# Performance work log

Measured on AMD Instinct MI355X. Metric: run time of the kernel, lower is better.

The kernel has to match this reference:

```python
import jax, jax.numpy as jnp
import numpy as np

N_NODES = 10000
N_EDGES = 320000
D = 128      # node/edge feature dim
H = 512      # MLP hidden width


def _mlp(x, W1, b1, W2, b2):
    return jax.nn.relu(x @ W1 + b1) @ W2 + b2


def setup_inputs() -> dict:
    key = jax.random.key(0)
    ks = jax.random.split(key, 8)
    s = lambda fan_in: 1.0 / np.sqrt(fan_in)
    return {
        "x": jax.random.normal(ks[0], (N_NODES, D), jnp.float32),
        "edge_index": jax.random.randint(ks[1], (2, N_EDGES), 0, N_NODES, jnp.int64),
        "edge_attr": jax.random.normal(ks[2], (N_EDGES, D), jnp.float32),
        "We1": jax.random.normal(ks[3], (3 * D, H), jnp.float32) * s(3 * D),
        "be1": jnp.zeros((H,), jnp.float32),
        "We2": jax.random.normal(ks[4], (H, D), jnp.float32) * s(H),
        "be2": jnp.zeros((D,), jnp.float32),
        "Wn1": jax.random.normal(ks[5], (2 * D, H), jnp.float32) * s(2 * D),
        "bn1": jnp.zeros((H,), jnp.float32),
        "Wn2": jax.random.normal(ks[6], (H, D), jnp.float32) * s(H),
        "bn2": jnp.zeros((D,), jnp.float32),
    }


def reference(x, edge_index, edge_attr, We1, be1, We2, be2, Wn1, bn1, Wn2, bn2):
    senders = edge_index[0]
    receivers = edge_index[1]
    # gather -> edge MLP
    edge_inputs = jnp.concatenate([x[senders], x[receivers], edge_attr], axis=-1)  # [E, 3D]
    updated_edge_attr = _mlp(edge_inputs, We1, be1, We2, be2)                      # [E, D]
    # scatter-add into receiving nodes
    aggregated = jax.ops.segment_sum(updated_edge_attr, receivers, num_segments=x.shape[0])  # [N, D]
    # node MLP
    node_inputs = jnp.concatenate([x, aggregated], axis=-1)                        # [N, 2D]
    updated_nodes = _mlp(node_inputs, Wn1, bn1, Wn2, bn2)                          # [N, D]
    return updated_nodes, updated_edge_attr
```

## Files before the change

### kernel.cpp

```cpp
#include <hip/hip_runtime.h>
#include <hip/hip_bf16.h>

#define N_NODES 10000
#define N_EDGES 320000
#define D 128
#define H 512

typedef __bf16 bf16x8 __attribute__((ext_vector_type(8)));
typedef float f32x4 __attribute__((ext_vector_type(4)));
typedef unsigned short u16x8 __attribute__((ext_vector_type(8)));

__device__ __forceinline__ unsigned short f2bf(float f) {
    union { float f; unsigned u; } v; v.f = f;
    unsigned r = v.u + 0x7fffu + ((v.u >> 16) & 1u);
    return (unsigned short)(r >> 16);
}

__global__ void cast_x_kernel(const float* __restrict__ x, unsigned short* __restrict__ xb) {
    int t = blockIdx.x * 256 + threadIdx.x;
    float4 v = reinterpret_cast<const float4*>(x)[t];
    ushort4 o;
    o.x = f2bf(v.x); o.y = f2bf(v.y); o.z = f2bf(v.z); o.w = f2bf(v.w);
    reinterpret_cast<ushort4*>(xb)[t] = o;
}

__global__ void swizzle_w_kernel(const float* __restrict__ W, unsigned short* __restrict__ out,
                                 int K, int Nn) {
    int t = blockIdx.x * 256 + threadIdx.x;
    int total = (K >> 5) * (Nn >> 4) * 64;
    if (t >= total) return;
    int lane = t & 63;
    int tile = t >> 6;
    int ntiles = Nn >> 4;
    int nt = tile % ntiles;
    int kt = tile / ntiles;
    int k0 = kt * 32 + (lane >> 4) * 8;
    int n  = nt * 16 + (lane & 15);
    unsigned short tmp[8];
#pragma unroll
    for (int j = 0; j < 8; ++j) tmp[j] = f2bf(W[(size_t)(k0 + j) * Nn + n]);
    ushort4* dst = reinterpret_cast<ushort4*>(out + (size_t)t * 8);
    dst[0] = *reinterpret_cast<ushort4*>(&tmp[0]);
    dst[1] = *reinterpret_cast<ushort4*>(&tmp[4]);
}

__global__ void hist_kernel(const int* __restrict__ eidx, int* __restrict__ deg) {
    int e = blockIdx.x * 256 + threadIdx.x;
    if (e < N_EDGES) atomicAdd(&deg[eidx[N_EDGES + e]], 1);
}

__global__ __launch_bounds__(1024) void scan_kernel(const int* __restrict__ deg,
                                                    int* __restrict__ rowstart,
                                                    int* __restrict__ cursor) {
    __shared__ int wsums[16];
    const int t = threadIdx.x;
    const int lane = t & 63, wv = t >> 6;
    const int base = t * 10;
    int loc[10];
    int s = 0;
#pragma unroll
    for (int i = 0; i < 10; ++i) {
        int v = (base + i < N_NODES) ? deg[base + i] : 0;
        loc[i] = s; s += v;
    }
    const int tot = s;
    int inc = tot;
#pragma unroll
    for (int d = 1; d < 64; d <<= 1) {
        int n = __shfl_up(inc, d, 64);
        if (lane >= d) inc += n;
    }
    if (lane == 63) wsums[wv] = inc;
    __syncthreads();
    if (t == 0) {
        int run = 0;
#pragma unroll
        for (int w = 0; w < 16; ++w) { int v = wsums[w]; wsums[w] = run; run += v; }
    }
    __syncthreads();
    const int off = wsums[wv] + inc - tot;
#pragma unroll
    for (int i = 0; i < 10; ++i) {
        int idx = base + i;
        if (idx < N_NODES) { int v = off + loc[i]; rowstart[idx] = v; cursor[idx] = v; }
    }
    if (t == 1023) rowstart[N_NODES] = off + tot;
}

__global__ void scatter_kernel(const int* __restrict__ eidx, int* __restrict__ cursor,
                               int* __restrict__ elist) {
    int e = blockIdx.x * 256 + threadIdx.x;
    if (e < N_EDGES) {
        int p = atomicAdd(&cursor[eidx[N_EDGES + e]], 1);
        elist[p] = e;
    }
}

__global__ __launch_bounds__(256, 2) void edge_mlp_kernel(
    const unsigned short* __restrict__ xb,
    const int* __restrict__ eidx,
    const float* __restrict__ edge_attr,
    const unsigned short* __restrict__ We1s,
    const float* __restrict__ be1,
    const unsigned short* __restrict__ We2s,
    const float* __restrict__ be2,
    float* __restrict__ out_edges)
{
    __shared__ unsigned short sA[64 * 392];
    __shared__ unsigned short sH[64 * 136];

    const int tid = threadIdx.x;
    const int wave = tid >> 6, lane = tid & 63;
    const int e0 = blockIdx.x * 64;
    const int l15 = lane & 15;
    const int q8 = (lane >> 4) * 8;

#pragma unroll
    for (int seg = 0; seg < 2; ++seg) {
        for (int c = tid; c < 1024; c += 256) {
            int row = c >> 4;
            int off = (c & 15) << 3;
            int e = e0 + row;
            int node = eidx[seg * N_EDGES + e];
            *reinterpret_cast<bf16x8*>(&sA[row * 392 + seg * 128 + off]) =
                *reinterpret_cast<const bf16x8*>(&xb[(size_t)node * 128 + off]);
        }
    }
    for (int c = tid; c < 1024; c += 256) {
        int row = c >> 4;
        int off = (c & 15) << 3;
        int e = e0 + row;
        const float4* src = reinterpret_cast<const float4*>(&edge_attr[(size_t)e * 128 + off]);
        float4 v0 = src[0], v1 = src[1];
        u16x8 o;
        o[0] = f2bf(v0.x); o[1] = f2bf(v0.y); o[2] = f2bf(v0.z); o[3] = f2bf(v0.w);
        o[4] = f2bf(v1.x); o[5] = f2bf(v1.y); o[6] = f2bf(v1.z); o[7] = f2bf(v1.w);
        *reinterpret_cast<u16x8*>(&sA[row * 392 + 256 + off]) = o;
    }
    __syncthreads();

    f32x4 acc1[8][4];
#pragma unroll
    for (int j = 0; j < 8; ++j)
#pragma unroll
        for (int mt = 0; mt < 4; ++mt) acc1[j][mt] = (f32x4){0.f, 0.f, 0.f, 0.f};
    f32x4 acc2[2][4];
#pragma unroll
    for (int nn = 0; nn < 2; ++nn)
#pragma unroll
        for (int mt = 0; mt < 4; ++mt) acc2[nn][mt] = (f32x4){0.f, 0.f, 0.f, 0.f};

#pragma unroll 2
    for (int kt = 0; kt < 12; ++kt) {
        bf16x8 a[4];
#pragma unroll
        for (int mt = 0; mt < 4; ++mt)
            a[mt] = *reinterpret_cast<const bf16x8*>(&sA[(mt * 16 + l15) * 392 + kt * 32 + q8]);
#pragma unroll
        for (int j = 0; j < 8; ++j) {
            int ntile = (j >> 1) * 8 + wave * 2 + (j & 1);
            bf16x8 b = *reinterpret_cast<const bf16x8*>(
                &We1s[(((size_t)kt * 32 + ntile) * 64 + lane) * 8]);
#pragma unroll
            for (int mt = 0; mt < 4; ++mt)
                acc1[j][mt] = __builtin_amdgcn_mfma_f32_16x16x32_bf16(a[mt], b, acc1[j][mt], 0, 0, 0);
        }
    }

#pragma unroll
    for (int h = 0; h < 4; ++h) {
        __syncthreads();
#pragma unroll
        for (int nn = 0; nn < 2; ++nn) {
            int cc = (wave * 2 + nn) * 16 + l15;
            float bias = be1[h * 128 + cc];
#pragma unroll
            for (int mt = 0; mt < 4; ++mt)
#pragma unroll
                for (int r = 0; r < 4; ++r) {
                    float v = acc1[h * 2 + nn][mt][r] + bias;
                    v = v > 0.f ? v : 0.f;
                    int row = mt * 16 + (lane >> 4) * 4 + r;
                    sH[row * 136 + cc] = f2bf(v);
                }
        }
        __syncthreads();

#pragma unroll
        for (int kt = 0; kt < 4; ++kt) {
            bf16x8 a[4];
#pragma unroll
            for (int mt = 0; mt < 4; ++mt)
                a[mt] = *reinterpret_cast<const bf16x8*>(&sH[(mt * 16 + l15) * 136 + kt * 32 + q8]);
#pragma unroll
            for (int nn = 0; nn < 2; ++nn) {
                int ntile = wave * 2 + nn;
                bf16x8 b = *reinterpret_cast<const bf16x8*>(
                    &We2s[(((size_t)(h * 4 + kt) * 8 + ntile) * 64 + lane) * 8]);
#pragma unroll
                for (int mt = 0; mt < 4; ++mt)
                    acc2[nn][mt] = __builtin_amdgcn_mfma_f32_16x16x32_bf16(a[mt], b, acc2[nn][mt], 0, 0, 0);
            }
        }
    }

#pragma unroll
    for (int nn = 0; nn < 2; ++nn) {
        int cc = (wave * 2 + nn) * 16 + l15;
        float bias = be2[cc];
#pragma unroll
        for (int mt = 0; mt < 4; ++mt)
#pragma unroll
            for (int r = 0; r < 4; ++r) {
                int row = mt * 16 + (lane >> 4) * 4 + r;
                out_edges[(size_t)(e0 + row) * 128 + cc] = acc2[nn][mt][r] + bias;
            }
    }
}

__global__ __launch_bounds__(256, 2) void node_mlp_kernel(
    const unsigned short* __restrict__ xb,
    const float* __restrict__ out_edges,
    const int* __restrict__ rowstart,
    const int* __restrict__ elist,
    const unsigned short* __restrict__ Wn1s,
    const float* __restrict__ bn1,
    const unsigned short* __restrict__ Wn2s,
    const float* __restrict__ bn2,
    float* __restrict__ out_nodes)
{
    __shared__ unsigned short sA[64 * 264];
    __shared__ unsigned short sH[64 * 136];

    const int tid = threadIdx.x;
    const int wave = tid >> 6, lane = tid & 63;
    const int n0 = blockIdx.x * 64;
    const int l15 = lane & 15;
    const int q8 = (lane >> 4) * 8;

    for (int c = tid; c < 1024; c += 256) {
        int row = c >> 4;
        int off = (c & 15) << 3;
        int node = n0 + row;
        bf16x8 v = {};
        if (node < N_NODES)
            v = *reinterpret_cast<const bf16x8*>(&xb[(size_t)node * 128 + off]);
        *reinterpret_cast<bf16x8*>(&sA[row * 264 + off]) = v;
    }

    {
        int row = tid >> 2, chunk = tid & 3;
        int node = n0 + row;
        f32x4 ag[8];
#pragma unroll
        for (int q = 0; q < 8; ++q) ag[q] = (f32x4){0.f, 0.f, 0.f, 0.f};
        if (node < N_NODES) {
            int r0 = rowstart[node], r1 = rowstart[node + 1];
            for (int j = r0; j < r1; ++j) {
                int e = elist[j];
                const f32x4* src =
                    reinterpret_cast<const f32x4*>(&out_edges[(size_t)e * 128 + chunk * 32]);
#pragma unroll
                for (int q = 0; q < 8; ++q) ag[q] += src[q];
            }
        }
#pragma unroll
        for (int q = 0; q < 4; ++q) {
            u16x8 o;
            o[0] = f2bf(ag[2 * q][0]); o[1] = f2bf(ag[2 * q][1]);
            o[2] = f2bf(ag[2 * q][2]); o[3] = f2bf(ag[2 * q][3]);
            o[4] = f2bf(ag[2 * q + 1][0]); o[5] = f2bf(ag[2 * q + 1][1]);
            o[6] = f2bf(ag[2 * q + 1][2]); o[7] = f2bf(ag[2 * q + 1][3]);
            *reinterpret_cast<u16x8*>(&sA[row * 264 + 128 + chunk * 32 + q * 8]) = o;
        }
    }
    __syncthreads();

    f32x4 acc1[8][4];
#pragma unroll
    for (int j = 0; j < 8; ++j)
#pragma unroll
        for (int mt = 0; mt < 4; ++mt) acc1[j][mt] = (f32x4){0.f, 0.f, 0.f, 0.f};
    f32x4 acc2[2][4];
#pragma unroll
    for (int nn = 0; nn < 2; ++nn)
#pragma unroll
        for (int mt = 0; mt < 4; ++mt) acc2[nn][mt] = (f32x4){0.f, 0.f, 0.f, 0.f};

#pragma unroll 2
    for (int kt = 0; kt < 8; ++kt) {
        bf16x8 a[4];
#pragma unroll
        for (int mt = 0; mt < 4; ++mt)
            a[mt] = *reinterpret_cast<const bf16x8*>(&sA[(mt * 16 + l15) * 264 + kt * 32 + q8]);
#pragma unroll
        for (int j = 0; j < 8; ++j) {
            int ntile = (j >> 1) * 8 + wave * 2 + (j & 1);
            bf16x8 b = *reinterpret_cast<const bf16x8*>(
                &Wn1s[(((size_t)kt * 32 + ntile) * 64 + lane) * 8]);
#pragma unroll
            for (int mt = 0; mt < 4; ++mt)
                acc1[j][mt] = __builtin_amdgcn_mfma_f32_16x16x32_bf16(a[mt], b, acc1[j][mt], 0, 0, 0);
        }
    }

#pragma unroll
    for (int h = 0; h < 4; ++h) {
        __syncthreads();
#pragma unroll
        for (int nn = 0; nn < 2; ++nn) {
            int cc = (wave * 2 + nn) * 16 + l15;
            float bias = bn1[h * 128 + cc];
#pragma unroll
            for (int mt = 0; mt < 4; ++mt)
#pragma unroll
                for (int r = 0; r < 4; ++r) {
                    float v = acc1[h * 2 + nn][mt][r] + bias;
                    v = v > 0.f ? v : 0.f;
                    int row = mt * 16 + (lane >> 4) * 4 + r;
                    sH[row * 136 + cc] = f2bf(v);
                }
        }
        __syncthreads();

#pragma unroll
        for (int kt = 0; kt < 4; ++kt) {
            bf16x8 a[4];
#pragma unroll
            for (int mt = 0; mt < 4; ++mt)
                a[mt] = *reinterpret_cast<const bf16x8*>(&sH[(mt * 16 + l15) * 136 + kt * 32 + q8]);
#pragma unroll
            for (int nn = 0; nn < 2; ++nn) {
                int ntile = wave * 2 + nn;
                bf16x8 b = *reinterpret_cast<const bf16x8*>(
                    &Wn2s[(((size_t)(h * 4 + kt) * 8 + ntile) * 64 + lane) * 8]);
#pragma unroll
                for (int mt = 0; mt < 4; ++mt)
                    acc2[nn][mt] = __builtin_amdgcn_mfma_f32_16x16x32_bf16(a[mt], b, acc2[nn][mt], 0, 0, 0);
            }
        }
    }

#pragma unroll
    for (int nn = 0; nn < 2; ++nn) {
        int cc = (wave * 2 + nn) * 16 + l15;
        float bias = bn2[cc];
#pragma unroll
        for (int mt = 0; mt < 4; ++mt)
#pragma unroll
            for (int r = 0; r < 4; ++r) {
                int row = mt * 16 + (lane >> 4) * 4 + r;
                int node = n0 + row;
                if (node < N_NODES)
                    out_nodes[(size_t)node * 128 + cc] = acc2[nn][mt][r] + bias;
            }
    }
}

extern "C" void kernel_launch(void* const* d_in, const int* in_sizes, int n_in,
                              void* d_out, int out_size, void* d_ws, size_t ws_size,
                              hipStream_t stream) {
    const float* x         = (const float*)d_in[0];
    const int*   eidx      = (const int*)d_in[1];
    const float* edge_attr = (const float*)d_in[2];
    const float* We1       = (const float*)d_in[3];
    const float* be1       = (const float*)d_in[4];
    const float* We2       = (const float*)d_in[5];
    const float* be2       = (const float*)d_in[6];
    const float* Wn1       = (const float*)d_in[7];
    const float* bn1       = (const float*)d_in[8];
    const float* Wn2       = (const float*)d_in[9];
    const float* bn2       = (const float*)d_in[10];
    float* out = (float*)d_out;

    char* ws = (char*)d_ws;
    size_t off = 0;
    auto alloc = [&](size_t bytes) {
        void* p = ws + off;
        off += (bytes + 255) & ~(size_t)255;
        return p;
    };
    unsigned short* xb   = (unsigned short*)alloc((size_t)N_NODES * D * 2);
    unsigned short* We1s = (unsigned short*)alloc((size_t)384 * 512 * 2);
    unsigned short* We2s = (unsigned short*)alloc((size_t)512 * 128 * 2);
    unsigned short* Wn1s = (unsigned short*)alloc((size_t)256 * 512 * 2);
    unsigned short* Wn2s = (unsigned short*)alloc((size_t)512 * 128 * 2);
    int* deg      = (int*)alloc((size_t)(N_NODES + 1) * 4);
    int* rowstart = (int*)alloc((size_t)(N_NODES + 1) * 4);
    int* cursor   = (int*)alloc((size_t)(N_NODES + 1) * 4);
    int* elist    = (int*)alloc((size_t)N_EDGES * 4);

    float* out_edges = out + (size_t)N_NODES * D;

    hipMemsetAsync(deg, 0, (size_t)N_NODES * sizeof(int), stream);
    cast_x_kernel<<<(N_NODES * D / 4 + 255) / 256, 256, 0, stream>>>(x, xb);
    swizzle_w_kernel<<<(12 * 32 * 64 + 255) / 256, 256, 0, stream>>>(We1, We1s, 384, 512);
    swizzle_w_kernel<<<(16 * 8 * 64 + 255) / 256, 256, 0, stream>>>(We2, We2s, 512, 128);
    swizzle_w_kernel<<<(8 * 32 * 64 + 255) / 256, 256, 0, stream>>>(Wn1, Wn1s, 256, 512);
    swizzle_w_kernel<<<(16 * 8 * 64 + 255) / 256, 256, 0, stream>>>(Wn2, Wn2s, 512, 128);

    hist_kernel<<<(N_EDGES + 255) / 256, 256, 0, stream>>>(eidx, deg);
    scan_kernel<<<1, 1024, 0, stream>>>(deg, rowstart, cursor);
    scatter_kernel<<<(N_EDGES + 255) / 256, 256, 0, stream>>>(eidx, cursor, elist);

    edge_mlp_kernel<<<N_EDGES / 64, 256, 0, stream>>>(
        xb, eidx, edge_attr, We1s, be1, We2s, be2, out_edges);
    node_mlp_kernel<<<(N_NODES + 63) / 64, 256, 0, stream>>>(
        xb, out_edges, rowstart, elist, Wn1s, bn1, Wn2s, bn2, out);
}
```

Baseline: 685.0 us.

## Double-buffer hidden tile in reused LDS and split aggregation into separate kernel

The edge and node MLP kernels now reuse the input tile's shared memory as two ping-pong hidden buffers. The ReLU write of the next hidden chunk overlaps with the second GEMM on the current chunk, which removes one barrier per chunk and lowers LDS use per block. The segment-sum aggregation moves out of the node MLP into a dedicated kernel with one wave per node. That kernel writes bf16 aggregates, which fixes the poor parallelism of the old four-threads-per-node gather, at the cost of an extra launch and an intermediate buffer.

```diff
diff --git a/kernel.cpp b/kernel.cpp
--- a/kernel.cpp
+++ b/kernel.cpp
@@ -96,6 +96,25 @@
     }
 }
 
+__global__ __launch_bounds__(256) void agg_kernel(
+    const float* __restrict__ out_edges,
+    const int* __restrict__ rowstart,
+    const int* __restrict__ elist,
+    unsigned short* __restrict__ aggb)
+{
+    int node = blockIdx.x * 4 + (threadIdx.x >> 6);
+    int lane = threadIdx.x & 63;
+    int r0 = rowstart[node], r1 = rowstart[node + 1];
+    float sx = 0.f, sy = 0.f;
+    for (int j = r0; j < r1; ++j) {
+        int e = elist[j];
+        float2 v = *reinterpret_cast<const float2*>(&out_edges[(size_t)e * 128 + lane * 2]);
+        sx += v.x; sy += v.y;
+    }
+    ushort2 o; o.x = f2bf(sx); o.y = f2bf(sy);
+    *reinterpret_cast<ushort2*>(&aggb[(size_t)node * 128 + lane * 2]) = o;
+}
+
 __global__ __launch_bounds__(256, 2) void edge_mlp_kernel(
     const unsigned short* __restrict__ xb,
     const int* __restrict__ eidx,
@@ -107,7 +126,8 @@
     float* __restrict__ out_edges)
 {
     __shared__ unsigned short sA[64 * 392];
-    __shared__ unsigned short sH[64 * 136];
+    unsigned short* const sH0 = sA;
+    unsigned short* const sH1 = sA + 64 * 136;
 
     const int tid = threadIdx.x;
     const int wave = tid >> 6, lane = tid & 63;
@@ -167,41 +187,56 @@
         }
     }
 
+#define WRITE_H(hh, dst, B1)                                                  \
+    {                                                                         \
+        _Pragma("unroll")                                                     \
+        for (int nn = 0; nn < 2; ++nn) {                                      \
+            int cc = (wave * 2 + nn) * 16 + l15;                              \
+            float bias = (B1)[(hh) * 128 + cc];                               \
+            _Pragma("unroll")                                                 \
+            for (int mt = 0; mt < 4; ++mt)                                    \
+                _Pragma("unroll")                                             \
+                for (int r = 0; r < 4; ++r) {                                 \
+                    float v = acc1[(hh) * 2 + nn][mt][r] + bias;              \
+                    v = v > 0.f ? v : 0.f;                                    \
+                    int row = mt * 16 + (lane >> 4) * 4 + r;                  \
+                    (dst)[row * 136 + cc] = f2bf(v);                          \
+                }                                                             \
+        }                                                                     \
+    }
+
+#define GEMM2_CHUNK(hh, src, W2)                                              \
+    {                                                                         \
+        _Pragma("unroll")                                                     \
+        for (int kt = 0; kt < 4; ++kt) {                                      \
+            bf16x8 a[4];                                                      \
+            _Pragma("unroll")                                                 \
+            for (int mt = 0; mt < 4; ++mt)                                    \
+                a[mt] = *reinterpret_cast<const bf16x8*>(                     \
+                    &(src)[(mt * 16 + l15) * 136 + kt * 32 + q8]);            \
+            _Pragma("unroll")                                                 \
+            for (int nn = 0; nn < 2; ++nn) {                                  \
+                int ntile = wave * 2 + nn;                                    \
+                bf16x8 b = *reinterpret_cast<const bf16x8*>(                  \
+                    &(W2)[(((size_t)((hh) * 4 + kt) * 8 + ntile) * 64 + lane) * 8]); \
+                _Pragma("unroll")                                             \
+                for (int mt = 0; mt < 4; ++mt)                                \
+                    acc2[nn][mt] = __builtin_amdgcn_mfma_f32_16x16x32_bf16(   \
+                        a[mt], b, acc2[nn][mt], 0, 0, 0);                     \
+            }                                                                 \
+        }                                                                     \
+    }
+
+    __syncthreads();
+    WRITE_H(0, sH0, be1);
+    __syncthreads();
 #pragma unroll
     for (int h = 0; h < 4; ++h) {
-        __syncthreads();
-#pragma unroll
-        for (int nn = 0; nn < 2; ++nn) {
-            int cc = (wave * 2 + nn) * 16 + l15;
-            float bias = be1[h * 128 + cc];
-#pragma unroll
-            for (int mt = 0; mt < 4; ++mt)
-#pragma unroll
-                for (int r = 0; r < 4; ++r) {
-                    float v = acc1[h * 2 + nn][mt][r] + bias;
-                    v = v > 0.f ? v : 0.f;
-                    int row = mt * 16 + (lane >> 4) * 4 + r;
-                    sH[row * 136 + cc] = f2bf(v);
-                }
-        }
-        __syncthreads();
-
-#pragma unroll
-        for (int kt = 0; kt < 4; ++kt) {
-            bf16x8 a[4];
-#pragma unroll
-            for (int mt = 0; mt < 4; ++mt)
-                a[mt] = *reinterpret_cast<const bf16x8*>(&sH[(mt * 16 + l15) * 136 + kt * 32 + q8]);
-#pragma unroll
-            for (int nn = 0; nn < 2; ++nn) {
-                int ntile = wave * 2 + nn;
-                bf16x8 b = *reinterpret_cast<const bf16x8*>(
-                    &We2s[(((size_t)(h * 4 + kt) * 8 + ntile) * 64 + lane) * 8]);
-#pragma unroll
-                for (int mt = 0; mt < 4; ++mt)
-                    acc2[nn][mt] = __builtin_amdgcn_mfma_f32_16x16x32_bf16(a[mt], b, acc2[nn][mt], 0, 0, 0);
-            }
-        }
+        unsigned short* const cur = (h & 1) ? sH1 : sH0;
+        unsigned short* const nxt = (h & 1) ? sH0 : sH1;
+        if (h < 3) WRITE_H(h + 1, nxt, be1);
+        GEMM2_CHUNK(h, cur, We2s);
+        if (h < 3) __syncthreads();
     }
 
 #pragma unroll
@@ -220,17 +255,16 @@
 
 __global__ __launch_bounds__(256, 2) void node_mlp_kernel(
     const unsigned short* __restrict__ xb,
-    const float* __restrict__ out_edges,
-    const int* __restrict__ rowstart,
-    const int* __restrict__ elist,
+    const unsigned short* __restrict__ aggb,
     const unsigned short* __restrict__ Wn1s,
     const float* __restrict__ bn1,
     const unsigned short* __restrict__ Wn2s,
     const float* __restrict__ bn2,
     float* __restrict__ out_nodes)
 {
-    __shared__ unsigned short sA[64 * 264];
-    __shared__ unsigned short sH[64 * 136];
+    __shared__ unsigned short sA[17408];
+    unsigned short* const sH0 = sA;
+    unsigned short* const sH1 = sA + 64 * 136;
 
     const int tid = threadIdx.x;
     const int wave = tid >> 6, lane = tid & 63;
@@ -247,32 +281,14 @@
             v = *reinterpret_cast<const bf16x8*>(&xb[(size_t)node * 128 + off]);
         *reinterpret_cast<bf16x8*>(&sA[row * 264 + off]) = v;
     }
-
-    {
-        int row = tid >> 2, chunk = tid & 3;
+    for (int c = tid; c < 1024; c += 256) {
+        int row = c >> 4;
+        int off = (c & 15) << 3;
         int node = n0 + row;
-        f32x4 ag[8];
-#pragma unroll
-        for (int q = 0; q < 8; ++q) ag[q] = (f32x4){0.f, 0.f, 0.f, 0.f};
-        if (node < N_NODES) {
-            int r0 = rowstart[node], r1 = rowstart[node + 1];
-            for (int j = r0; j < r1; ++j) {
-                int e = elist[j];
-                const f32x4* src =
-                    reinterpret_cast<const f32x4*>(&out_edges[(size_t)e * 128 + chunk * 32]);
-#pragma unroll
-                for (int q = 0; q < 8; ++q) ag[q] += src[q];
-            }
-        }
-#pragma unroll
-        for (int q = 0; q < 4; ++q) {
-            u16x8 o;
-            o[0] = f2bf(ag[2 * q][0]); o[1] = f2bf(ag[2 * q][1]);
-            o[2] = f2bf(ag[2 * q][2]); o[3] = f2bf(ag[2 * q][3]);
-            o[4] = f2bf(ag[2 * q + 1][0]); o[5] = f2bf(ag[2 * q + 1][1]);
-            o[6] = f2bf(ag[2 * q + 1][2]); o[7] = f2bf(ag[2 * q + 1][3]);
-            *reinterpret_cast<u16x8*>(&sA[row * 264 + 128 + chunk * 32 + q * 8]) = o;
-        }
+        bf16x8 v = {};
+        if (node < N_NODES)
+            v = *reinterpret_cast<const bf16x8*>(&aggb[(size_t)node * 128 + off]);
+        *reinterpret_cast<bf16x8*>(&sA[row * 264 + 128 + off]) = v;
     }
     __syncthreads();
 
@@ -304,41 +320,16 @@
         }
     }
 
+    __syncthreads();
+    WRITE_H(0, sH0, bn1);
+    __syncthreads();
 #pragma unroll
     for (int h = 0; h < 4; ++h) {
-        __syncthreads();
-#pragma unroll
-        for (int nn = 0; nn < 2; ++nn) {
-            int cc = (wave * 2 + nn) * 16 + l15;
-            float bias = bn1[h * 128 + cc];
-#pragma unroll
-            for (int mt = 0; mt < 4; ++mt)
-#pragma unroll
-                for (int r = 0; r < 4; ++r) {
-                    float v = acc1[h * 2 + nn][mt][r] + bias;
-                    v = v > 0.f ? v : 0.f;
-                    int row = mt * 16 + (lane >> 4) * 4 + r;
-                    sH[row * 136 + cc] = f2bf(v);
-                }
-        }
-        __syncthreads();
-
-#pragma unroll
-        for (int kt = 0; kt < 4; ++kt) {
-            bf16x8 a[4];
-#pragma unroll
-            for (int mt = 0; mt < 4; ++mt)
-                a[mt] = *reinterpret_cast<const bf16x8*>(&sH[(mt * 16 + l15) * 136 + kt * 32 + q8]);
-#pragma unroll
-            for (int nn = 0; nn < 2; ++nn) {
-                int ntile = wave * 2 + nn;
-                bf16x8 b = *reinterpret_cast<const bf16x8*>(
-                    &Wn2s[(((size_t)(h * 4 + kt) * 8 + ntile) * 64 + lane) * 8]);
-#pragma unroll
-                for (int mt = 0; mt < 4; ++mt)
-                    acc2[nn][mt] = __builtin_amdgcn_mfma_f32_16x16x32_bf16(a[mt], b, acc2[nn][mt], 0, 0, 0);
-            }
-        }
+        unsigned short* const cur = (h & 1) ? sH1 : sH0;
+        unsigned short* const nxt = (h & 1) ? sH0 : sH1;
+        if (h < 3) WRITE_H(h + 1, nxt, bn1);
+        GEMM2_CHUNK(h, cur, Wn2s);
+        if (h < 3) __syncthreads();
     }
 
 #pragma unroll
@@ -385,6 +376,7 @@
     unsigned short* We2s = (unsigned short*)alloc((size_t)512 * 128 * 2);
     unsigned short* Wn1s = (unsigned short*)alloc((size_t)256 * 512 * 2);
     unsigned short* Wn2s = (unsigned short*)alloc((size_t)512 * 128 * 2);
+    unsigned short* aggb = (unsigned short*)alloc((size_t)N_NODES * D * 2);
     int* deg      = (int*)alloc((size_t)(N_NODES + 1) * 4);
     int* rowstart = (int*)alloc((size_t)(N_NODES + 1) * 4);
     int* cursor   = (int*)alloc((size_t)(N_NODES + 1) * 4);
@@ -405,6 +397,7 @@
 
     edge_mlp_kernel<<<N_EDGES / 64, 256, 0, stream>>>(
         xb, eidx, edge_attr, We1s, be1, We2s, be2, out_edges);
+    agg_kernel<<<N_NODES / 4, 256, 0, stream>>>(out_edges, rowstart, elist, aggb);
     node_mlp_kernel<<<(N_NODES + 63) / 64, 256, 0, stream>>>(
-        xb, out_edges, rowstart, elist, Wn1s, bn1, Wn2s, bn2, out);
-}
+        xb, aggb, Wn1s, bn1, Wn2s, bn2, out);
+}
```

Result: no change. 690.5 us (+0.8%).
